# Optimization experiments

Hardware: AMD Instinct MI355X
Metric: run time of the kernel (lower is better)

The kernel has to match this reference:

```python
import jax, jax.numpy as jnp
import numpy as np

M_MARGIN = 0.25
GAMMA = 256.0
NEG_INF = jnp.float32(-1e30)


def setup_inputs() -> dict:
    key = jax.random.key(0)
    k1, k2 = jax.random.split(key)
    feature = jax.random.normal(k1, (8192, 128), dtype=jnp.float32)
    label = jax.random.randint(k2, (8192,), 0, 64, dtype=jnp.int64)
    return {"feature": feature, "label": label}


def reference(feature, label):
    # F.normalize: L2-normalize rows (eps=1e-12)
    norm = jnp.maximum(jnp.linalg.norm(feature, axis=1, keepdims=True), 1e-12)
    f = feature / norm
    sim = f @ f.T  # [N, N]
    N = sim.shape[0]

    same = label[:, None] == label[None, :]
    triu = jnp.triu(jnp.ones((N, N), dtype=bool), k=1)
    pos_mask = same & triu
    neg_mask = (~same) & triu

    sim_d = jax.lax.stop_gradient(sim)  # .detach() in original
    ap = jnp.maximum(-sim_d + 1.0 + M_MARGIN, 0.0)
    an = jnp.maximum(sim_d + M_MARGIN, 0.0)
    delta_p = 1.0 - M_MARGIN
    delta_n = M_MARGIN

    logit_p = -ap * (sim - delta_p) * GAMMA
    logit_n = an * (sim - delta_n) * GAMMA

    # boolean-gather + logsumexp == masked logsumexp (fixed shapes, jit-friendly)
    lse_p = jax.nn.logsumexp(jnp.where(pos_mask, logit_p, NEG_INF))
    lse_n = jax.nn.logsumexp(jnp.where(neg_mask, logit_n, NEG_INF))

    return jax.nn.softplus(lse_n + lse_p)
```

## Files before the change

kernel.cpp:

```cpp
#include <hip/hip_runtime.h>
#include <hip/hip_bf16.h>
#include <math.h>

#define NROW 8192
#define DIM  128
#define BM   64
#define BN   128
#define NTILES 4160
#define NT4    (NTILES * 4)
#define NRED   32
#define PERRED (NT4 / NRED)

typedef __bf16 bf16x8 __attribute__((ext_vector_type(8)));
typedef float  f32x4  __attribute__((ext_vector_type(4)));
typedef float  f32x2  __attribute__((ext_vector_type(2)));

#define G2      369.3299304675746f
#define NEGBIG  (-3.0e38f)
#define NOFF    2000.0f

__global__ __launch_bounds__(256)
void prep_kernel(const float* __restrict__ f, __hip_bfloat16* __restrict__ fhi) {
    int row  = blockIdx.x * 4 + (threadIdx.x >> 6);
    int lane = threadIdx.x & 63;
    float2 v = ((const float2*)(f + (size_t)row * DIM))[lane];
    float ss = v.x * v.x + v.y * v.y;
    #pragma unroll
    for (int off = 32; off; off >>= 1) ss += __shfl_xor(ss, off, 64);
    float inv = 1.0f / fmaxf(sqrtf(ss), 1e-12f);
    __hip_bfloat162 hv;
    hv.x = __float2bfloat16(v.x * inv);
    hv.y = __float2bfloat16(v.y * inv);
    ((__hip_bfloat162*)(fhi + (size_t)row * DIM))[lane] = hv;
}

__device__ __forceinline__ int tstart(int tr) {
    int m = tr >> 1;
    int f = m * m - ((tr & 1) ? 0 : m);
    return 64 * tr - f;
}

__global__ __launch_bounds__(256, 4)
void sim_kernel(const __hip_bfloat16* __restrict__ fhi,
                const int* __restrict__ lab,
                float4* __restrict__ blockRes) {
    const int tid  = threadIdx.x;
    const int w    = tid >> 6;
    const int lane = tid & 63;
    const int lrow = lane & 15;
    const int lk   = lane >> 4;

    int bid = blockIdx.x;
    float sa = fmaxf(16384.f - 4.f * (float)bid, 0.f);
    int tr = 128 - (int)sqrtf(sa);
    if (tr > 127) tr = 127;
    if (tr < 0) tr = 0;
    while (tr > 0 && bid < tstart(tr)) --tr;
    while (bid >= tstart(tr + 1)) ++tr;
    const int tc = (tr >> 1) + (bid - tstart(tr));

    const int rowBase = tr * BM;
    const int colBase = tc * BN;

    __shared__ __align__(16) char smem[24 * 1024];
    __shared__ int labA[BM];
    __shared__ int labB[BN];

    if (tid < BM)            labA[tid] = lab[rowBase + tid];
    else if (tid < BM + BN)  labB[tid - BM] = lab[colBase + (tid - BM)];

    f32x4 acc[4][2];
    #pragma unroll
    for (int mi = 0; mi < 4; ++mi)
        #pragma unroll
        for (int ni = 0; ni < 2; ++ni) acc[mi][ni] = (f32x4){0.f, 0.f, 0.f, 0.f};

    const int ncol0 = w * 32;
    const int rsub = lane >> 3;
    const int kbs  = 16 * ((lane & 7) ^ rsub);

    for (int kc = 0; kc < 2; ++kc) {
        #pragma unroll
        for (int t = 0; t < 6; ++t) {
            int seg = w * 6 + t;
            char* ldsb = smem + seg * 1024;
            int grow = (seg < 8) ? (rowBase + (seg & 7) * 8 + rsub)
                                 : (colBase + (seg - 8) * 8 + rsub);
            const char* g = (const char*)fhi + (size_t)grow * 256 + kc * 128 + kbs;
            __builtin_amdgcn_global_load_lds(
                (const __attribute__((address_space(1))) void*)g,
                (__attribute__((address_space(3))) void*)ldsb, 16, 0, 0);
        }
        __syncthreads();

        const char* As = smem;
        const char* Bs = smem + 8192;
        #pragma unroll
        for (int c = 0; c < 2; ++c) {
            int kb = c * 64 + lk * 16;
            bf16x8 bfr[2];
            #pragma unroll
            for (int ni = 0; ni < 2; ++ni) {
                int rb = ncol0 + ni * 16 + lrow;
                bfr[ni] = *(const bf16x8*)(Bs + rb * 128 + (kb ^ ((rb & 7) << 4)));
            }
            #pragma unroll
            for (int mi = 0; mi < 4; ++mi) {
                int ra = mi * 16 + lrow;
                bf16x8 afr = *(const bf16x8*)(As + ra * 128 + (kb ^ ((ra & 7) << 4)));
                #pragma unroll
                for (int ni = 0; ni < 2; ++ni)
                    acc[mi][ni] = __builtin_amdgcn_mfma_f32_16x16x32_bf16(afr, bfr[ni], acc[mi][ni], 0, 0, 0);
            }
        }
        if (kc == 0) __syncthreads();
    }

    const f32x2 G2v   = {G2, G2};
    const f32x2 Pposv = {-2.0f * G2, -2.0f * G2};
    const f32x2 Qposv = {0.9375f * G2, 0.9375f * G2};
    const f32x2 Qnegv = {-0.0625f * G2 - NOFF, -0.0625f * G2 - NOFF};
    const f32x2 mq    = {-0.25f, -0.25f};
    float mall = NEGBIG, mneg = NEGBIG;

    int lbv[2];
    #pragma unroll
    for (int ni = 0; ni < 2; ++ni) lbv[ni] = labB[ncol0 + ni * 16 + lrow];

#define PASS_A(EDGEF)                                                          \
    _Pragma("unroll")                                                          \
    for (int mi = 0; mi < 4; ++mi) {                                           \
        int4 la4 = *(const int4*)&labA[mi * 16 + lk * 4];                      \
        const int la[4] = {la4.x, la4.y, la4.z, la4.w};                        \
        _Pragma("unroll")                                                      \
        for (int ni = 0; ni < 2; ++ni) {                                       \
            const int lb = lbv[ni];                                            \
            f32x4 v = acc[mi][ni];                                             \
            f32x2 s01 = {v.x, v.y}, s23 = {v.z, v.w};                          \
            f32x2 xp01 = __builtin_elementwise_fma(G2v, s01 * s01,             \
                           __builtin_elementwise_fma(Pposv, s01, Qposv));      \
            f32x2 xp23 = __builtin_elementwise_fma(G2v, s23 * s23,             \
                           __builtin_elementwise_fma(Pposv, s23, Qposv));      \
            f32x2 t01 = __builtin_elementwise_max(s01, mq);                    \
            f32x2 t23 = __builtin_elementwise_max(s23, mq);                    \
            f32x2 xn01 = __builtin_elementwise_fma(G2v, t01 * t01, Qnegv);     \
            f32x2 xn23 = __builtin_elementwise_fma(G2v, t23 * t23, Qnegv);     \
            const float xpv[4] = {xp01.x, xp01.y, xp23.x, xp23.y};             \
            const float xnv[4] = {xn01.x, xn01.y, xn23.x, xn23.y};             \
            _Pragma("unroll")                                                  \
            for (int r = 0; r < 4; ++r) {                                      \
                bool pos = (la[r] == lb);                                      \
                float x = pos ? xpv[r] : xnv[r];                               \
                if (EDGEF) {                                                   \
                    int ig = rowBase + mi * 16 + lk * 4 + r;                   \
                    int jg = colBase + ncol0 + ni * 16 + lrow;                 \
                    x = (jg > ig) ? x : NEGBIG;                                \
                }                                                              \
                mall = fmaxf(mall, x);                                         \
                mneg = fmaxf(mneg, pos ? NEGBIG : x);                          \
                acc[mi][ni][r] = x;                                            \
            }                                                                  \
        }                                                                      \
    }

    if (tc == (tr >> 1)) { PASS_A(true) } else { PASS_A(false) }
#undef PASS_A

    #pragma unroll
    for (int off = 32; off; off >>= 1) {
        mall = fmaxf(mall, __shfl_xor(mall, off, 64));
        mneg = fmaxf(mneg, __shfl_xor(mneg, off, 64));
    }
    const float Mp  = (mall > -1000.f) ? mall : 0.f;
    const float Mn2 = (mneg > -2500.f) ? mneg : -4000.f;

    const f32x2 Mpv = {Mp, Mp}, Mnv = {Mn2, Mn2};
    f32x2 sp2 = {0.f, 0.f}, sn2 = {0.f, 0.f};
    #pragma unroll
    for (int mi = 0; mi < 4; ++mi)
        #pragma unroll
        for (int ni = 0; ni < 2; ++ni) {
            f32x4 v = acc[mi][ni];
            #pragma unroll
            for (int h = 0; h < 2; ++h) {
                f32x2 p = h ? (f32x2){v.z, v.w} : (f32x2){v.x, v.y};
                f32x2 dp = p - Mpv;
                sp2 += (f32x2){__builtin_amdgcn_exp2f(dp.x),
                               __builtin_amdgcn_exp2f(dp.y)};
                float xm0 = (p.x > -1000.f) ? NEGBIG : p.x;
                float xm1 = (p.y > -1000.f) ? NEGBIG : p.y;
                f32x2 dn = (f32x2){xm0, xm1} - Mnv;
                sn2 += (f32x2){__builtin_amdgcn_exp2f(dn.x),
                               __builtin_amdgcn_exp2f(dn.y)};
            }
        }
    float sp = sp2.x + sp2.y, sn = sn2.x + sn2.y;

    #pragma unroll
    for (int off = 32; off; off >>= 1) {
        sp += __shfl_xor(sp, off, 64);
        sn += __shfl_xor(sn, off, 64);
    }
    if (lane == 0) blockRes[bid * 4 + w] = make_float4(Mp, sp, Mn2, sn);
}

__device__ __forceinline__ void merge2(float& m, float& s, float mo, float so) {
    float M = fmaxf(m, mo);
    s = s * __builtin_amdgcn_exp2f(m - M) + so * __builtin_amdgcn_exp2f(mo - M);
    m = M;
}

__global__ __launch_bounds__(256)
void reduce_kernel(const float4* __restrict__ in, float4* __restrict__ partial) {
    __shared__ float red[4][4];
    const int tid  = threadIdx.x;
    const int base = blockIdx.x * PERRED;
    float mp = NEGBIG, sp = 0.f, mn = NEGBIG, sn = 0.f;
    for (int i = tid; i < PERRED; i += 256) {
        float4 v = in[base + i];
        merge2(mp, sp, v.x, v.y);
        merge2(mn, sn, v.z, v.w);
    }
    #pragma unroll
    for (int off = 32; off; off >>= 1) {
        float mo = __shfl_xor(mp, off, 64), so = __shfl_xor(sp, off, 64);
        merge2(mp, sp, mo, so);
        float mo2 = __shfl_xor(mn, off, 64), so2 = __shfl_xor(sn, off, 64);
        merge2(mn, sn, mo2, so2);
    }
    const int wv = tid >> 6;
    if ((tid & 63) == 0) {
        red[wv][0] = mp; red[wv][1] = sp; red[wv][2] = mn; red[wv][3] = sn;
    }
    __syncthreads();
    if (tid == 0) {
        mp = red[0][0]; sp = red[0][1]; mn = red[0][2]; sn = red[0][3];
        #pragma unroll
        for (int q = 1; q < 4; ++q) {
            merge2(mp, sp, red[q][0], red[q][1]);
            merge2(mn, sn, red[q][2], red[q][3]);
        }
        partial[blockIdx.x] = make_float4(mp, sp, mn, sn);
    }
}

__global__ __launch_bounds__(64)
void finalize_kernel(const float4* __restrict__ partial, float* __restrict__ out) {
    const int lane = threadIdx.x;
    float mp = NEGBIG, sp = 0.f, mn = NEGBIG, sn = 0.f;
    if (lane < NRED) {
        float4 v = partial[lane];
        mp = v.x; sp = v.y; mn = v.z; sn = v.w;
    }
    #pragma unroll
    for (int off = 32; off; off >>= 1) {
        float mo = __shfl_xor(mp, off, 64), so = __shfl_xor(sp, off, 64);
        merge2(mp, sp, mo, so);
        float mo2 = __shfl_xor(mn, off, 64), so2 = __shfl_xor(sn, off, 64);
        merge2(mn, sn, mo2, so2);
    }
    if (lane == 0) {
        const double LN2 = 0.6931471805599453;
        double lse_p = ((double)mp + log2((double)sp)) * LN2;
        double lse_n = ((double)mn + (double)NOFF + log2((double)sn)) * LN2;
        double xx = lse_p + lse_n;
        double r = (xx > 30.0) ? xx : log1p(exp(xx));
        out[0] = (float)r;
    }
}

extern "C" void kernel_launch(void* const* d_in, const int* in_sizes, int n_in,
                              void* d_out, int out_size, void* d_ws, size_t ws_size,
                              hipStream_t stream) {
    const float* f   = (const float*)d_in[0];
    const int*   lab = (const int*)d_in[1];
    float*  out      = (float*)d_out;

    __hip_bfloat16* fhi = (__hip_bfloat16*)d_ws;
    float4* blockRes    = (float4*)((char*)d_ws + 4u * 1024 * 1024);
    float4* partial     = (float4*)((char*)d_ws + 8u * 1024 * 1024);

    prep_kernel<<<NROW / 4, 256, 0, stream>>>(f, fhi);
    sim_kernel<<<NTILES, 256, 0, stream>>>(fhi, lab, blockRes);
    reduce_kernel<<<NRED, 256, 0, stream>>>(blockRes, partial);
    finalize_kernel<<<1, 64, 0, stream>>>(partial, out);
}
```

Measured before the change: 44.72 us.

## Sort rows by label so most tiles take a negatives-only epilogue

A histogram and prefix-sum kernel is added, and prep scatters the normalized rows and their labels into label-sorted order. Since the pair set is symmetric, relabelling the rows leaves the result unchanged. Most sim tiles then contain no same-label pairs and run a fast path with one exp per element, no label compares, and an analytic max derived from max |t|. Mixed tiles also compute their maxima analytically and use one exp per element instead of two. The cost is an extra single-block kernel launch, atomic scatter in prep, and a nondeterministic row order.

```diff
diff --git a/kernel.cpp b/kernel.cpp
--- a/kernel.cpp
+++ b/kernel.cpp
@@ -13,14 +13,40 @@
 
 typedef __bf16 bf16x8 __attribute__((ext_vector_type(8)));
 typedef float  f32x4  __attribute__((ext_vector_type(4)));
-typedef float  f32x2  __attribute__((ext_vector_type(2)));
-
-#define G2      369.3299304675746f
-#define NEGBIG  (-3.0e38f)
-#define NOFF    2000.0f
+
+#define G2     369.3299304675746f
+#define QPOS   (0.9375f * G2)
+#define QNEG   (-0.0625f * G2)
+#define NEGBIG (-3.0e38f)
+#define MSENT  (-4000.0f)
 
 __global__ __launch_bounds__(256)
-void prep_kernel(const float* __restrict__ f, __hip_bfloat16* __restrict__ fhi) {
+void hist_kernel(const int* __restrict__ lab, int* __restrict__ cursor) {
+    __shared__ int h[4][64];
+    const int tid  = threadIdx.x;
+    const int w    = tid >> 6;
+    const int lane = tid & 63;
+    h[w][lane] = 0;
+    __syncthreads();
+    for (int i = tid; i < NROW; i += 256)
+        atomicAdd(&h[w][lab[i]], 1);
+    __syncthreads();
+    if (tid < 64) {
+        int tot = h[0][tid] + h[1][tid] + h[2][tid] + h[3][tid];
+        int v = tot;
+        #pragma unroll
+        for (int off = 1; off < 64; off <<= 1) {
+            int u = __shfl_up(v, off, 64);
+            if (tid >= off) v += u;
+        }
+        cursor[tid] = v - tot;
+    }
+}
+
+__global__ __launch_bounds__(256)
+void prep_kernel(const float* __restrict__ f, const int* __restrict__ lab,
+                 int* __restrict__ cursor,
+                 __hip_bfloat16* __restrict__ fhi, int* __restrict__ labS) {
     int row  = blockIdx.x * 4 + (threadIdx.x >> 6);
     int lane = threadIdx.x & 63;
     float2 v = ((const float2*)(f + (size_t)row * DIM))[lane];
@@ -28,10 +54,15 @@
     #pragma unroll
     for (int off = 32; off; off >>= 1) ss += __shfl_xor(ss, off, 64);
     float inv = 1.0f / fmaxf(sqrtf(ss), 1e-12f);
+    int l = lab[row];
+    int dest = 0;
+    if (lane == 0) dest = atomicAdd(&cursor[l], 1);
+    dest = __shfl(dest, 0, 64);
     __hip_bfloat162 hv;
     hv.x = __float2bfloat16(v.x * inv);
     hv.y = __float2bfloat16(v.y * inv);
-    ((__hip_bfloat162*)(fhi + (size_t)row * DIM))[lane] = hv;
+    ((__hip_bfloat162*)(fhi + (size_t)dest * DIM))[lane] = hv;
+    if (lane == 0) labS[dest] = l;
 }
 
 __device__ __forceinline__ int tstart(int tr) {
@@ -42,7 +73,7 @@
 
 __global__ __launch_bounds__(256, 4)
 void sim_kernel(const __hip_bfloat16* __restrict__ fhi,
-                const int* __restrict__ lab,
+                const int* __restrict__ labS,
                 float4* __restrict__ blockRes) {
     const int tid  = threadIdx.x;
     const int w    = tid >> 6;
@@ -62,12 +93,17 @@
     const int rowBase = tr * BM;
     const int colBase = tc * BN;
 
+    const int labRowEnd = labS[rowBase + BM - 1];
+    const int labCol0   = labS[colBase];
+    const bool edge  = (tc == (tr >> 1));
+    const bool mixed = edge || (labRowEnd == labCol0);
+
     __shared__ __align__(16) char smem[24 * 1024];
     __shared__ int labA[BM];
     __shared__ int labB[BN];
 
-    if (tid < BM)            labA[tid] = lab[rowBase + tid];
-    else if (tid < BM + BN)  labB[tid - BM] = lab[colBase + (tid - BM)];
+    if (tid < BM)            labA[tid] = labS[rowBase + tid];
+    else if (tid < BM + BN)  labB[tid - BM] = labS[colBase + (tid - BM)];
 
     f32x4 acc[4][2];
     #pragma unroll
@@ -116,92 +152,123 @@
         if (kc == 0) __syncthreads();
     }
 
-    const f32x2 G2v   = {G2, G2};
-    const f32x2 Pposv = {-2.0f * G2, -2.0f * G2};
-    const f32x2 Qposv = {0.9375f * G2, 0.9375f * G2};
-    const f32x2 Qnegv = {-0.0625f * G2 - NOFF, -0.0625f * G2 - NOFF};
-    const f32x2 mq    = {-0.25f, -0.25f};
-    float mall = NEGBIG, mneg = NEGBIG;
-
-    int lbv[2];
-    #pragma unroll
-    for (int ni = 0; ni < 2; ++ni) lbv[ni] = labB[ncol0 + ni * 16 + lrow];
-
-#define PASS_A(EDGEF)                                                          \
+    float4 res;
+    if (!mixed) {
+        float mx = 0.0f;
+        #pragma unroll
+        for (int mi = 0; mi < 4; ++mi)
+            #pragma unroll
+            for (int ni = 0; ni < 2; ++ni)
+                #pragma unroll
+                for (int r = 0; r < 4; ++r) {
+                    float t = fmaxf(acc[mi][ni][r], -0.25f);
+                    acc[mi][ni][r] = t;
+                    mx = fmaxf(mx, fabsf(t));
+                }
+        #pragma unroll
+        for (int off = 32; off; off >>= 1)
+            mx = fmaxf(mx, __shfl_xor(mx, off, 64));
+        const float zc = -G2 * mx * mx;
+        float sn = 0.f;
+        #pragma unroll
+        for (int mi = 0; mi < 4; ++mi)
+            #pragma unroll
+            for (int ni = 0; ni < 2; ++ni)
+                #pragma unroll
+                for (int r = 0; r < 4; ++r) {
+                    float t = acc[mi][ni][r];
+                    sn += __builtin_amdgcn_exp2f(fmaf(G2, t * t, zc));
+                }
+        #pragma unroll
+        for (int off = 32; off; off >>= 1)
+            sn += __shfl_xor(sn, off, 64);
+        res = make_float4(MSENT, 0.f, fmaf(G2, mx * mx, QNEG), sn);
+    } else {
+        float minp = 1e30f;
+        float mabs = -1.0f;
+        int lbv[2];
+        #pragma unroll
+        for (int ni = 0; ni < 2; ++ni) lbv[ni] = labB[ncol0 + ni * 16 + lrow];
+
+#define PASS_AB(EDGEF)                                                         \
     _Pragma("unroll")                                                          \
     for (int mi = 0; mi < 4; ++mi) {                                           \
         int4 la4 = *(const int4*)&labA[mi * 16 + lk * 4];                      \
         const int la[4] = {la4.x, la4.y, la4.z, la4.w};                        \
         _Pragma("unroll")                                                      \
         for (int ni = 0; ni < 2; ++ni) {                                       \
-            const int lb = lbv[ni];                                            \
-            f32x4 v = acc[mi][ni];                                             \
-            f32x2 s01 = {v.x, v.y}, s23 = {v.z, v.w};                          \
-            f32x2 xp01 = __builtin_elementwise_fma(G2v, s01 * s01,             \
-                           __builtin_elementwise_fma(Pposv, s01, Qposv));      \
-            f32x2 xp23 = __builtin_elementwise_fma(G2v, s23 * s23,             \
-                           __builtin_elementwise_fma(Pposv, s23, Qposv));      \
-            f32x2 t01 = __builtin_elementwise_max(s01, mq);                    \
-            f32x2 t23 = __builtin_elementwise_max(s23, mq);                    \
-            f32x2 xn01 = __builtin_elementwise_fma(G2v, t01 * t01, Qnegv);     \
-            f32x2 xn23 = __builtin_elementwise_fma(G2v, t23 * t23, Qnegv);     \
-            const float xpv[4] = {xp01.x, xp01.y, xp23.x, xp23.y};             \
-            const float xnv[4] = {xn01.x, xn01.y, xn23.x, xn23.y};             \
             _Pragma("unroll")                                                  \
             for (int r = 0; r < 4; ++r) {                                      \
-                bool pos = (la[r] == lb);                                      \
-                float x = pos ? xpv[r] : xnv[r];                               \
+                float s = acc[mi][ni][r];                                      \
+                bool pos = (la[r] == lbv[ni]);                                 \
+                float t = fmaxf(s, -0.25f);                                    \
+                bool valid = true;                                             \
                 if (EDGEF) {                                                   \
                     int ig = rowBase + mi * 16 + lk * 4 + r;                   \
                     int jg = colBase + ncol0 + ni * 16 + lrow;                 \
-                    x = (jg > ig) ? x : NEGBIG;                                \
+                    valid = (jg > ig);                                         \
+                    pos = pos && valid;                                        \
                 }                                                              \
-                mall = fmaxf(mall, x);                                         \
-                mneg = fmaxf(mneg, pos ? NEGBIG : x);                          \
-                acc[mi][ni][r] = x;                                            \
+                float u = pos ? s : t;                                         \
+                minp = fminf(minp, pos ? s : 1e30f);                           \
+                bool nm = EDGEF ? (valid && !pos) : !pos;                      \
+                mabs = fmaxf(mabs, nm ? fabsf(t) : -1.0f);                     \
+                acc[mi][ni][r] = u;                                            \
             }                                                                  \
         }                                                                      \
     }
-
-    if (tc == (tr >> 1)) { PASS_A(true) } else { PASS_A(false) }
-#undef PASS_A
-
-    #pragma unroll
-    for (int off = 32; off; off >>= 1) {
-        mall = fmaxf(mall, __shfl_xor(mall, off, 64));
-        mneg = fmaxf(mneg, __shfl_xor(mneg, off, 64));
-    }
-    const float Mp  = (mall > -1000.f) ? mall : 0.f;
-    const float Mn2 = (mneg > -2500.f) ? mneg : -4000.f;
-
-    const f32x2 Mpv = {Mp, Mp}, Mnv = {Mn2, Mn2};
-    f32x2 sp2 = {0.f, 0.f}, sn2 = {0.f, 0.f};
-    #pragma unroll
-    for (int mi = 0; mi < 4; ++mi)
-        #pragma unroll
-        for (int ni = 0; ni < 2; ++ni) {
-            f32x4 v = acc[mi][ni];
-            #pragma unroll
-            for (int h = 0; h < 2; ++h) {
-                f32x2 p = h ? (f32x2){v.z, v.w} : (f32x2){v.x, v.y};
-                f32x2 dp = p - Mpv;
-                sp2 += (f32x2){__builtin_amdgcn_exp2f(dp.x),
-                               __builtin_amdgcn_exp2f(dp.y)};
-                float xm0 = (p.x > -1000.f) ? NEGBIG : p.x;
-                float xm1 = (p.y > -1000.f) ? NEGBIG : p.y;
-                f32x2 dn = (f32x2){xm0, xm1} - Mnv;
-                sn2 += (f32x2){__builtin_amdgcn_exp2f(dn.x),
-                               __builtin_amdgcn_exp2f(dn.y)};
-            }
-        }
-    float sp = sp2.x + sp2.y, sn = sn2.x + sn2.y;
-
-    #pragma unroll
-    for (int off = 32; off; off >>= 1) {
-        sp += __shfl_xor(sp, off, 64);
-        sn += __shfl_xor(sn, off, 64);
-    }
-    if (lane == 0) blockRes[bid * 4 + w] = make_float4(Mp, sp, Mn2, sn);
+        if (edge) { PASS_AB(true) } else { PASS_AB(false) }
+#undef PASS_AB
+
+        #pragma unroll
+        for (int off = 32; off; off >>= 1) {
+            minp = fminf(minp, __shfl_xor(minp, off, 64));
+            mabs = fmaxf(mabs, __shfl_xor(mabs, off, 64));
+        }
+        const float Mp = (minp < 2.0f)
+            ? fmaf(G2, minp * minp, fmaf(-2.0f * G2, minp, QPOS)) : MSENT;
+        const float Mn = (mabs >= 0.0f) ? fmaf(G2, mabs * mabs, QNEG) : MSENT;
+        const float qph = QPOS - Mp;
+        const float qnh = QNEG - Mn;
+        float sp = 0.f, sn = 0.f;
+
+#define PASS_B(EDGEF)                                                          \
+    _Pragma("unroll")                                                          \
+    for (int mi = 0; mi < 4; ++mi) {                                           \
+        int4 la4 = *(const int4*)&labA[mi * 16 + lk * 4];                      \
+        const int la[4] = {la4.x, la4.y, la4.z, la4.w};                        \
+        _Pragma("unroll")                                                      \
+        for (int ni = 0; ni < 2; ++ni) {                                       \
+            _Pragma("unroll")                                                  \
+            for (int r = 0; r < 4; ++r) {                                      \
+                float u = acc[mi][ni][r];                                      \
+                bool pos = (la[r] == lbv[ni]);                                 \
+                float P  = pos ? (-2.0f * G2) : 0.0f;                          \
+                float Qh = pos ? qph : qnh;                                    \
+                float e = __builtin_amdgcn_exp2f(                              \
+                              fmaf(G2, u * u, fmaf(P, u, Qh)));                \
+                if (EDGEF) {                                                   \
+                    int ig = rowBase + mi * 16 + lk * 4 + r;                   \
+                    int jg = colBase + ncol0 + ni * 16 + lrow;                 \
+                    e = (jg > ig) ? e : 0.f;                                   \
+                }                                                              \
+                float ep = pos ? e : 0.f;                                      \
+                sp += ep;                                                      \
+                sn += (e - ep);                                                \
+            }                                                                  \
+        }                                                                      \
+    }
+        if (edge) { PASS_B(true) } else { PASS_B(false) }
+#undef PASS_B
+
+        #pragma unroll
+        for (int off = 32; off; off >>= 1) {
+            sp += __shfl_xor(sp, off, 64);
+            sn += __shfl_xor(sn, off, 64);
+        }
+        res = make_float4(Mp, sp, Mn, sn);
+    }
+    if (lane == 0) blockRes[bid * 4 + w] = res;
 }
 
 __device__ __forceinline__ void merge2(float& m, float& s, float mo, float so) {
@@ -262,7 +329,7 @@
     if (lane == 0) {
         const double LN2 = 0.6931471805599453;
         double lse_p = ((double)mp + log2((double)sp)) * LN2;
-        double lse_n = ((double)mn + (double)NOFF + log2((double)sn)) * LN2;
+        double lse_n = ((double)mn + log2((double)sn)) * LN2;
         double xx = lse_p + lse_n;
         double r = (xx > 30.0) ? xx : log1p(exp(xx));
         out[0] = (float)r;
@@ -277,11 +344,14 @@
     float*  out      = (float*)d_out;
 
     __hip_bfloat16* fhi = (__hip_bfloat16*)d_ws;
-    float4* blockRes    = (float4*)((char*)d_ws + 4u * 1024 * 1024);
-    float4* partial     = (float4*)((char*)d_ws + 8u * 1024 * 1024);
-
-    prep_kernel<<<NROW / 4, 256, 0, stream>>>(f, fhi);
-    sim_kernel<<<NTILES, 256, 0, stream>>>(fhi, lab, blockRes);
+    int* labS    = (int*)((char*)d_ws + 2u * 1024 * 1024);
+    int* cursor  = (int*)((char*)d_ws + 3u * 1024 * 1024);
+    float4* blockRes = (float4*)((char*)d_ws + 4u * 1024 * 1024);
+    float4* partial  = (float4*)((char*)d_ws + 8u * 1024 * 1024);
+
+    hist_kernel<<<1, 256, 0, stream>>>(lab, cursor);
+    prep_kernel<<<NROW / 4, 256, 0, stream>>>(f, lab, cursor, fhi, labS);
+    sim_kernel<<<NTILES, 256, 0, stream>>>(fhi, labS, blockRes);
     reduce_kernel<<<NRED, 256, 0, stream>>>(blockRes, partial);
     finalize_kernel<<<1, 64, 0, stream>>>(partial, out);
 }
```

New measurement: 79.68 us. +78.2%, slower.
